# Optimization experiments

Hardware: AMD Instinct MI355X
Metric: run time of the kernel (lower is better)

The kernel has to match this reference:

```python
import jax, jax.numpy as jnp
import numpy as np

ALPHA = 0.2      # LeakyReLU negative slope
NEG_INF = -9e15  # mask value from the original module
EPS = 1e-8


def setup_inputs() -> dict:
    key = jax.random.key(0)
    k1, k2, k3, k4 = jax.random.split(key, 4)
    B, N, F_in, F_out = 8, 2048, 128, 64
    h = jax.random.normal(k1, (B, N, F_in), dtype=jnp.float32)
    u = jax.random.uniform(k2, (B, N, N), dtype=jnp.float32)
    adj = jnp.where(u > 0.9, u, 0.0)
    adj = jnp.maximum(adj, jnp.eye(N, dtype=jnp.float32)[None])
    # Xavier-uniform with gain 1.414 as in the torch init
    gain = 1.414
    bW = gain * np.sqrt(6.0 / (F_in + F_out))
    W = jax.random.uniform(k3, (F_in, F_out), jnp.float32, -bW, bW)
    ba = gain * np.sqrt(6.0 / (2 * F_out + 1))
    a = jax.random.uniform(k4, (2 * F_out, 1), jnp.float32, -ba, ba)
    return {"h": h, "adj": adj, "W": W, "a": a}


def reference(h, adj, W, a):
    # h: [B,N,Fin], adj: [B,N,N], W: [Fin,Fout], a: [2*Fout,1]
    F_out = W.shape[1]
    Wh = jnp.einsum('bnf,fo->bno', h, W)                      # [B,N,Fout]
    # Split-projection equivalent of cat([Wh_i, Wh_j]) @ a:
    # e[b,i,j] = leaky(Wh[b,i]@a1 + Wh[b,j]@a2)
    a1 = a[:F_out, 0]
    a2 = a[F_out:, 0]
    e = jax.nn.leaky_relu(
        (Wh @ a1)[:, :, None] + (Wh @ a2)[:, None, :],        # [B,N,N]
        negative_slope=ALPHA,
    )
    att = jnp.where(adj > 0, e, NEG_INF)
    att = jax.nn.softmax(att, axis=2)
    att = att * adj
    att = att / (jnp.sum(att, axis=2, keepdims=True) + EPS)
    h_prime = jnp.einsum('bij,bjo->bio', att, Wh)             # [B,N,Fout]
    return jax.nn.elu(h_prime)                                # concat=True -> ELU
```

## Files before the change

### kernel.cpp

```cpp
#include <hip/hip_runtime.h>
#include <hip/hip_bf16.h>
#include <stdint.h>

#define LRELU_ALPHA 0.2f

constexpr int BB = 8, NN = 2048, FIN = 128, FOUT = 64;
constexpr int GEMM_ROWS = 32;
constexpr int NBLK_G = BB * NN / GEMM_ROWS;

typedef __attribute__((ext_vector_type(8))) short short8;
typedef __attribute__((ext_vector_type(4))) float f32x4;
typedef __attribute__((ext_vector_type(2))) float f32x2;

__device__ __forceinline__ ushort bf16rn(float f) {
    __hip_bfloat16 h = __float2bfloat16(f);
    return *reinterpret_cast<ushort*>(&h);
}

#define HS 132
__global__ __launch_bounds__(256) void k_gemm_hw(const float* __restrict__ h,
                                                 const float* __restrict__ W,
                                                 const float* __restrict__ a,
                                                 ushort* __restrict__ WhP,
                                                 float* __restrict__ s1,
                                                 float* __restrict__ s2,
                                                 float* __restrict__ pmax) {
    __shared__ float hs[GEMM_ROWS * HS];
    __shared__ __align__(16) ushort fragbuf[2048];
    __shared__ float smax[16];
    const int tid = threadIdx.x;
    const int base = blockIdx.x * GEMM_ROWS;

    #pragma unroll
    for (int rep = 0; rep < 4; ++rep) {
        int flat4 = rep * 256 + tid;
        int row = flat4 >> 5, k4 = flat4 & 31;
        float4 v = *reinterpret_cast<const float4*>(h + (size_t)(base + row) * FIN + k4 * 4);
        *reinterpret_cast<float4*>(&hs[row * HS + k4 * 4]) = v;
    }
    __syncthreads();

    const int tr = tid >> 4;
    const int tc = tid & 15;
    float acc[2][4] = {};
    #pragma unroll 4
    for (int k = 0; k < FIN; ++k) {
        float4 wv = *reinterpret_cast<const float4*>(W + (size_t)k * FOUT + tc * 4);
        #pragma unroll
        for (int r = 0; r < 2; ++r) {
            float hv = hs[(tr * 2 + r) * HS + k];
            acc[r][0] = fmaf(hv, wv.x, acc[r][0]);
            acc[r][1] = fmaf(hv, wv.y, acc[r][1]);
            acc[r][2] = fmaf(hv, wv.z, acc[r][2]);
            acc[r][3] = fmaf(hv, wv.w, acc[r][3]);
        }
    }

    #pragma unroll
    for (int r = 0; r < 2; ++r) {
        const int jloc = tr * 2 + r;
        const int e = jloc & 7, kgrp = jloc >> 3;
        #pragma unroll
        for (int c = 0; c < 4; ++c) {
            const int col = tc * 4 + c;
            fragbuf[((col >> 4) * 64 + kgrp * 16 + (col & 15)) * 8 + e] = bf16rn(acc[r][c]);
        }
    }

    float a1c[4], a2c[4];
    #pragma unroll
    for (int c = 0; c < 4; ++c) {
        a1c[c] = a[tc * 4 + c];
        a2c[c] = a[FOUT + tc * 4 + c];
    }
    float maxp2 = -3.4e38f;
    #pragma unroll
    for (int r = 0; r < 2; ++r) {
        float p1 = acc[r][0] * a1c[0] + acc[r][1] * a1c[1] + acc[r][2] * a1c[2] + acc[r][3] * a1c[3];
        float p2 = acc[r][0] * a2c[0] + acc[r][1] * a2c[1] + acc[r][2] * a2c[2] + acc[r][3] * a2c[3];
        #pragma unroll
        for (int off = 1; off < 16; off <<= 1) {
            p1 += __shfl_xor(p1, off);
            p2 += __shfl_xor(p2, off);
        }
        if (tc == 0) {
            s1[base + tr * 2 + r] = p1;
            s2[base + tr * 2 + r] = p2;
            maxp2 = fmaxf(maxp2, p2);
        }
    }
    if (tc == 0) smax[tr] = maxp2;
    __syncthreads();

    const size_t region = ((size_t)((base >> 11) * 64 + ((base & 2047) >> 5))) * 2048;
    *reinterpret_cast<uint4*>(WhP + region + tid * 8) =
        *reinterpret_cast<const uint4*>(fragbuf + tid * 8);

    if (tid == 0) {
        float mm = smax[0];
        #pragma unroll
        for (int i = 1; i < 16; ++i) mm = fmaxf(mm, smax[i]);
        pmax[blockIdx.x] = mm;
    }
}

__device__ __forceinline__ uint32_t wvpk(float ax, float ay, float px, float py,
                                         float nx, float ny, float e1p, float e1n) {
    f32x2 t1 = f32x2{e1p, e1p} * f32x2{px, py};
    f32x2 t2 = f32x2{e1n, e1n} * f32x2{nx, ny};
    f32x2 mx = {fmaxf(t1.x, t2.x), fmaxf(t1.y, t2.y)};
    f32x2 w2 = f32x2{ax, ay} * mx;
    uint32_t u0 = __float_as_uint(w2.x) + 0x8000u;
    uint32_t u1 = __float_as_uint(w2.y) + 0x8000u;
    return __builtin_amdgcn_perm(u1, u0, 0x07060302);
}

__global__ __launch_bounds__(256, 4) void k_attn(const float* __restrict__ adj,
                                                 const ushort* __restrict__ WhP,
                                                 const float* __restrict__ s1,
                                                 const float* __restrict__ s2,
                                                 const float* __restrict__ pmax,
                                                 float* __restrict__ out) {
    __shared__ float e2p[NN];
    __shared__ float e2n[NN];
    __shared__ float lacc[4][16][68];
    __shared__ float lS[4][16];

    const int tid = threadIdx.x;
    const int l = tid & 63, w = tid >> 6;
    const int li = l & 15, lk = l >> 4;
    const int blk = blockIdx.x;
    const int b = blk >> 7;
    const int rowbase = blk * 16;
    const int row_i = rowbase + li;

    float m = -3.4e38f;
    #pragma unroll
    for (int t = 0; t < 8; ++t) m = fmaxf(m, pmax[l + 64 * t]);
    #pragma unroll
    for (int off = 32; off > 0; off >>= 1) m = fmaxf(m, __shfl_xor(m, off));

    const float* __restrict__ s2B = s2 + (size_t)b * NN;
    #pragma unroll
    for (int k = 0; k < 8; ++k) {
        const int j = k * 256 + tid;
        const float d = s2B[j] - m;
        e2p[j] = __expf(d);
        e2n[j] = __expf(LRELU_ALPHA * d);
    }

    const float s1i = s1[row_i];
    const float cp = s1i + m;
    const float e1p = __expf(0.8f * fminf(cp, 0.f));
    const float e1n = __expf(-0.8f * fmaxf(cp, 0.f));

    __syncthreads();

    const float* __restrict__ adjp = adj + (size_t)row_i * NN + w * 512 + lk * 8;
    const ushort* __restrict__ whp = WhP + (size_t)b * 131072 + (size_t)(w * 16) * 2048 + l * 8;
    const float* __restrict__ e2pw = e2p + w * 512 + lk * 8;
    const float* __restrict__ e2nw = e2n + w * 512 + lk * 8;

    f32x4 acc0 = {0.f, 0.f, 0.f, 0.f};
    f32x4 acc1 = {0.f, 0.f, 0.f, 0.f};
    f32x4 acc2 = {0.f, 0.f, 0.f, 0.f};
    f32x4 acc3 = {0.f, 0.f, 0.f, 0.f};
    f32x4 accS = {0.f, 0.f, 0.f, 0.f};
    short8 ones;
    #pragma unroll
    for (int e = 0; e < 8; ++e) ones[e] = (short)0x3F80;

    float4 a0 = *reinterpret_cast<const float4*>(adjp);
    float4 a1 = *reinterpret_cast<const float4*>(adjp + 4);
    short8 b0 = *reinterpret_cast<const short8*>(whp);
    short8 b1 = *reinterpret_cast<const short8*>(whp + 512);
    short8 b2 = *reinterpret_cast<const short8*>(whp + 1024);
    short8 b3 = *reinterpret_cast<const short8*>(whp + 1536);

    #pragma unroll 2
    for (int t = 0; t < 16; ++t) {
        const int tn = (t < 15) ? t + 1 : 15;
        float4 na0 = *reinterpret_cast<const float4*>(adjp + tn * 32);
        float4 na1 = *reinterpret_cast<const float4*>(adjp + tn * 32 + 4);
        const ushort* np = whp + tn * 2048;
        short8 nb0 = *reinterpret_cast<const short8*>(np);
        short8 nb1 = *reinterpret_cast<const short8*>(np + 512);
        short8 nb2 = *reinterpret_cast<const short8*>(np + 1024);
        short8 nb3 = *reinterpret_cast<const short8*>(np + 1536);

        const float4* pp = reinterpret_cast<const float4*>(e2pw + t * 32);
        const float4* nn = reinterpret_cast<const float4*>(e2nw + t * 32);
        const float4 p0 = pp[0], p1 = pp[1];
        const float4 n0 = nn[0], n1 = nn[1];

        const uint32_t pk0 = wvpk(a0.x, a0.y, p0.x, p0.y, n0.x, n0.y, e1p, e1n);
        const uint32_t pk1 = wvpk(a0.z, a0.w, p0.z, p0.w, n0.z, n0.w, e1p, e1n);
        const uint32_t pk2 = wvpk(a1.x, a1.y, p1.x, p1.y, n1.x, n1.y, e1p, e1n);
        const uint32_t pk3 = wvpk(a1.z, a1.w, p1.z, p1.w, n1.z, n1.w, e1p, e1n);
        int4 afw = make_int4((int)pk0, (int)pk1, (int)pk2, (int)pk3);
        short8 af = *reinterpret_cast<short8*>(&afw);

        acc0 = __builtin_amdgcn_mfma_f32_16x16x32_bf16(af, b0, acc0, 0, 0, 0);
        acc1 = __builtin_amdgcn_mfma_f32_16x16x32_bf16(af, b1, acc1, 0, 0, 0);
        acc2 = __builtin_amdgcn_mfma_f32_16x16x32_bf16(af, b2, acc2, 0, 0, 0);
        acc3 = __builtin_amdgcn_mfma_f32_16x16x32_bf16(af, b3, acc3, 0, 0, 0);
        accS = __builtin_amdgcn_mfma_f32_16x16x32_bf16(af, ones, accS, 0, 0, 0);

        a0 = na0; a1 = na1;
        b0 = nb0; b1 = nb1; b2 = nb2; b3 = nb3;
    }

    if (li == 0) {
        #pragma unroll
        for (int r = 0; r < 4; ++r) lS[w][lk * 4 + r] = accS[r];
    }
    #pragma unroll
    for (int r = 0; r < 4; ++r) {
        lacc[w][lk * 4 + r][0 * 16 + li] = acc0[r];
        lacc[w][lk * 4 + r][1 * 16 + li] = acc1[r];
        lacc[w][lk * 4 + r][2 * 16 + li] = acc2[r];
        lacc[w][lk * 4 + r][3 * 16 + li] = acc3[r];
    }
    __syncthreads();

    #pragma unroll
    for (int q = 0; q < 4; ++q) {
        const int idx = q * 256 + tid;
        const int row = idx >> 6, col = idx & 63;
        float v = lacc[0][row][col] + lacc[1][row][col] + lacc[2][row][col] + lacc[3][row][col];
        float S = lS[0][row] + lS[1][row] + lS[2][row] + lS[3][row];
        float o = v / S;
        o = o > 0.f ? o : expm1f(o);
        out[(size_t)(rowbase + row) * FOUT + col] = o;
    }
}

extern "C" void kernel_launch(void* const* d_in, const int* in_sizes, int n_in,
                              void* d_out, int out_size, void* d_ws, size_t ws_size,
                              hipStream_t stream) {
    (void)in_sizes; (void)n_in; (void)out_size; (void)ws_size;
    const float* h   = (const float*)d_in[0];
    const float* adj = (const float*)d_in[1];
    const float* W   = (const float*)d_in[2];
    const float* a   = (const float*)d_in[3];
    float* out = (float*)d_out;

    ushort* WhP = (ushort*)d_ws;
    float* s1w  = (float*)(WhP + (size_t)BB * NN * FOUT);
    float* s2w  = s1w + (size_t)BB * NN;
    float* pmaxw = s2w + (size_t)BB * NN;

    k_gemm_hw<<<NBLK_G, 256, 0, stream>>>(h, W, a, WhP, s1w, s2w, pmaxw);
    k_attn<<<BB * NN / 16, 256, 0, stream>>>(adj, WhP, s1w, s2w, pmaxw, out);
}
```

Baseline: 45.55 us.

## Process 32 rows per attention block and stagger start tile per block

Each attention block now handles two 16-row groups, so each loaded Wh tile and the exp tables built in shared memory serve twice as many rows. This halves the number of blocks and the per-block setup of the e2p/e2n tables. The loop start is also rotated per block so concurrent blocks hit different Wh and adj regions. The cost is more registers and LDS per block, which may reduce occupancy, and fewer blocks in flight.

```diff
diff --git a/kernel.cpp b/kernel.cpp
--- a/kernel.cpp
+++ b/kernel.cpp
@@ -123,16 +123,17 @@
                                                  float* __restrict__ out) {
     __shared__ float e2p[NN];
     __shared__ float e2n[NN];
-    __shared__ float lacc[4][16][68];
-    __shared__ float lS[4][16];
+    __shared__ float lacc[4][32][68];
+    __shared__ float lS[4][32];
 
     const int tid = threadIdx.x;
     const int l = tid & 63, w = tid >> 6;
     const int li = l & 15, lk = l >> 4;
     const int blk = blockIdx.x;
-    const int b = blk >> 7;
-    const int rowbase = blk * 16;
-    const int row_i = rowbase + li;
+    const int b = blk >> 6;
+    const int rowbase = blk * 32;
+    const int rowA = rowbase + li;
+    const int rowB = rowbase + 16 + li;
 
     float m = -3.4e38f;
     #pragma unroll
@@ -149,82 +150,111 @@
         e2n[j] = __expf(LRELU_ALPHA * d);
     }
 
-    const float s1i = s1[row_i];
-    const float cp = s1i + m;
-    const float e1p = __expf(0.8f * fminf(cp, 0.f));
-    const float e1n = __expf(-0.8f * fmaxf(cp, 0.f));
-
-    __syncthreads();
-
-    const float* __restrict__ adjp = adj + (size_t)row_i * NN + w * 512 + lk * 8;
+    const float cpA = s1[rowA] + m;
+    const float e1pA = __expf(0.8f * fminf(cpA, 0.f));
+    const float e1nA = __expf(-0.8f * fmaxf(cpA, 0.f));
+    const float cpB = s1[rowB] + m;
+    const float e1pB = __expf(0.8f * fminf(cpB, 0.f));
+    const float e1nB = __expf(-0.8f * fmaxf(cpB, 0.f));
+
+    __syncthreads();
+
+    const float* __restrict__ adjA = adj + (size_t)rowA * NN + w * 512 + lk * 8;
+    const float* __restrict__ adjB = adj + (size_t)rowB * NN + w * 512 + lk * 8;
     const ushort* __restrict__ whp = WhP + (size_t)b * 131072 + (size_t)(w * 16) * 2048 + l * 8;
     const float* __restrict__ e2pw = e2p + w * 512 + lk * 8;
     const float* __restrict__ e2nw = e2n + w * 512 + lk * 8;
 
-    f32x4 acc0 = {0.f, 0.f, 0.f, 0.f};
-    f32x4 acc1 = {0.f, 0.f, 0.f, 0.f};
-    f32x4 acc2 = {0.f, 0.f, 0.f, 0.f};
-    f32x4 acc3 = {0.f, 0.f, 0.f, 0.f};
-    f32x4 accS = {0.f, 0.f, 0.f, 0.f};
+    f32x4 acc0a = {0,0,0,0}, acc1a = {0,0,0,0}, acc2a = {0,0,0,0}, acc3a = {0,0,0,0};
+    f32x4 acc0b = {0,0,0,0}, acc1b = {0,0,0,0}, acc2b = {0,0,0,0}, acc3b = {0,0,0,0};
+    f32x4 accSa = {0,0,0,0}, accSb = {0,0,0,0};
     short8 ones;
     #pragma unroll
     for (int e = 0; e < 8; ++e) ones[e] = (short)0x3F80;
 
-    float4 a0 = *reinterpret_cast<const float4*>(adjp);
-    float4 a1 = *reinterpret_cast<const float4*>(adjp + 4);
-    short8 b0 = *reinterpret_cast<const short8*>(whp);
-    short8 b1 = *reinterpret_cast<const short8*>(whp + 512);
-    short8 b2 = *reinterpret_cast<const short8*>(whp + 1024);
-    short8 b3 = *reinterpret_cast<const short8*>(whp + 1536);
-
+    const int off0 = (blk * 5) & 15;
+
+    float4 aA0 = *reinterpret_cast<const float4*>(adjA + off0 * 32);
+    float4 aA1 = *reinterpret_cast<const float4*>(adjA + off0 * 32 + 4);
+    float4 aB0 = *reinterpret_cast<const float4*>(adjB + off0 * 32);
+    float4 aB1 = *reinterpret_cast<const float4*>(adjB + off0 * 32 + 4);
+    short8 b0 = *reinterpret_cast<const short8*>(whp + off0 * 2048);
+    short8 b1 = *reinterpret_cast<const short8*>(whp + off0 * 2048 + 512);
+    short8 b2 = *reinterpret_cast<const short8*>(whp + off0 * 2048 + 1024);
+    short8 b3 = *reinterpret_cast<const short8*>(whp + off0 * 2048 + 1536);
+
+    int tt = off0;
     #pragma unroll 2
     for (int t = 0; t < 16; ++t) {
-        const int tn = (t < 15) ? t + 1 : 15;
-        float4 na0 = *reinterpret_cast<const float4*>(adjp + tn * 32);
-        float4 na1 = *reinterpret_cast<const float4*>(adjp + tn * 32 + 4);
+        const int tn = (tt + 1) & 15;
+        float4 nA0 = *reinterpret_cast<const float4*>(adjA + tn * 32);
+        float4 nA1 = *reinterpret_cast<const float4*>(adjA + tn * 32 + 4);
+        float4 nB0 = *reinterpret_cast<const float4*>(adjB + tn * 32);
+        float4 nB1 = *reinterpret_cast<const float4*>(adjB + tn * 32 + 4);
         const ushort* np = whp + tn * 2048;
         short8 nb0 = *reinterpret_cast<const short8*>(np);
         short8 nb1 = *reinterpret_cast<const short8*>(np + 512);
         short8 nb2 = *reinterpret_cast<const short8*>(np + 1024);
         short8 nb3 = *reinterpret_cast<const short8*>(np + 1536);
 
-        const float4* pp = reinterpret_cast<const float4*>(e2pw + t * 32);
-        const float4* nn = reinterpret_cast<const float4*>(e2nw + t * 32);
+        const float4* pp = reinterpret_cast<const float4*>(e2pw + tt * 32);
+        const float4* nn = reinterpret_cast<const float4*>(e2nw + tt * 32);
         const float4 p0 = pp[0], p1 = pp[1];
         const float4 n0 = nn[0], n1 = nn[1];
 
-        const uint32_t pk0 = wvpk(a0.x, a0.y, p0.x, p0.y, n0.x, n0.y, e1p, e1n);
-        const uint32_t pk1 = wvpk(a0.z, a0.w, p0.z, p0.w, n0.z, n0.w, e1p, e1n);
-        const uint32_t pk2 = wvpk(a1.x, a1.y, p1.x, p1.y, n1.x, n1.y, e1p, e1n);
-        const uint32_t pk3 = wvpk(a1.z, a1.w, p1.z, p1.w, n1.z, n1.w, e1p, e1n);
-        int4 afw = make_int4((int)pk0, (int)pk1, (int)pk2, (int)pk3);
-        short8 af = *reinterpret_cast<short8*>(&afw);
-
-        acc0 = __builtin_amdgcn_mfma_f32_16x16x32_bf16(af, b0, acc0, 0, 0, 0);
-        acc1 = __builtin_amdgcn_mfma_f32_16x16x32_bf16(af, b1, acc1, 0, 0, 0);
-        acc2 = __builtin_amdgcn_mfma_f32_16x16x32_bf16(af, b2, acc2, 0, 0, 0);
-        acc3 = __builtin_amdgcn_mfma_f32_16x16x32_bf16(af, b3, acc3, 0, 0, 0);
-        accS = __builtin_amdgcn_mfma_f32_16x16x32_bf16(af, ones, accS, 0, 0, 0);
-
-        a0 = na0; a1 = na1;
+        uint32_t k0, k1, k2, k3;
+        k0 = wvpk(aA0.x, aA0.y, p0.x, p0.y, n0.x, n0.y, e1pA, e1nA);
+        k1 = wvpk(aA0.z, aA0.w, p0.z, p0.w, n0.z, n0.w, e1pA, e1nA);
+        k2 = wvpk(aA1.x, aA1.y, p1.x, p1.y, n1.x, n1.y, e1pA, e1nA);
+        k3 = wvpk(aA1.z, aA1.w, p1.z, p1.w, n1.z, n1.w, e1pA, e1nA);
+        int4 afwA = make_int4((int)k0, (int)k1, (int)k2, (int)k3);
+        short8 afA = *reinterpret_cast<short8*>(&afwA);
+
+        k0 = wvpk(aB0.x, aB0.y, p0.x, p0.y, n0.x, n0.y, e1pB, e1nB);
+        k1 = wvpk(aB0.z, aB0.w, p0.z, p0.w, n0.z, n0.w, e1pB, e1nB);
+        k2 = wvpk(aB1.x, aB1.y, p1.x, p1.y, n1.x, n1.y, e1pB, e1nB);
+        k3 = wvpk(aB1.z, aB1.w, p1.z, p1.w, n1.z, n1.w, e1pB, e1nB);
+        int4 afwB = make_int4((int)k0, (int)k1, (int)k2, (int)k3);
+        short8 afB = *reinterpret_cast<short8*>(&afwB);
+
+        acc0a = __builtin_amdgcn_mfma_f32_16x16x32_bf16(afA, b0, acc0a, 0, 0, 0);
+        acc0b = __builtin_amdgcn_mfma_f32_16x16x32_bf16(afB, b0, acc0b, 0, 0, 0);
+        acc1a = __builtin_amdgcn_mfma_f32_16x16x32_bf16(afA, b1, acc1a, 0, 0, 0);
+        acc1b = __builtin_amdgcn_mfma_f32_16x16x32_bf16(afB, b1, acc1b, 0, 0, 0);
+        acc2a = __builtin_amdgcn_mfma_f32_16x16x32_bf16(afA, b2, acc2a, 0, 0, 0);
+        acc2b = __builtin_amdgcn_mfma_f32_16x16x32_bf16(afB, b2, acc2b, 0, 0, 0);
+        acc3a = __builtin_amdgcn_mfma_f32_16x16x32_bf16(afA, b3, acc3a, 0, 0, 0);
+        acc3b = __builtin_amdgcn_mfma_f32_16x16x32_bf16(afB, b3, acc3b, 0, 0, 0);
+        accSa = __builtin_amdgcn_mfma_f32_16x16x32_bf16(afA, ones, accSa, 0, 0, 0);
+        accSb = __builtin_amdgcn_mfma_f32_16x16x32_bf16(afB, ones, accSb, 0, 0, 0);
+
+        aA0 = nA0; aA1 = nA1; aB0 = nB0; aB1 = nB1;
         b0 = nb0; b1 = nb1; b2 = nb2; b3 = nb3;
+        tt = tn;
     }
 
     if (li == 0) {
         #pragma unroll
-        for (int r = 0; r < 4; ++r) lS[w][lk * 4 + r] = accS[r];
+        for (int r = 0; r < 4; ++r) {
+            lS[w][lk * 4 + r] = accSa[r];
+            lS[w][16 + lk * 4 + r] = accSb[r];
+        }
     }
     #pragma unroll
     for (int r = 0; r < 4; ++r) {
-        lacc[w][lk * 4 + r][0 * 16 + li] = acc0[r];
-        lacc[w][lk * 4 + r][1 * 16 + li] = acc1[r];
-        lacc[w][lk * 4 + r][2 * 16 + li] = acc2[r];
-        lacc[w][lk * 4 + r][3 * 16 + li] = acc3[r];
-    }
-    __syncthreads();
-
-    #pragma unroll
-    for (int q = 0; q < 4; ++q) {
+        lacc[w][lk * 4 + r][0 * 16 + li] = acc0a[r];
+        lacc[w][lk * 4 + r][1 * 16 + li] = acc1a[r];
+        lacc[w][lk * 4 + r][2 * 16 + li] = acc2a[r];
+        lacc[w][lk * 4 + r][3 * 16 + li] = acc3a[r];
+        lacc[w][16 + lk * 4 + r][0 * 16 + li] = acc0b[r];
+        lacc[w][16 + lk * 4 + r][1 * 16 + li] = acc1b[r];
+        lacc[w][16 + lk * 4 + r][2 * 16 + li] = acc2b[r];
+        lacc[w][16 + lk * 4 + r][3 * 16 + li] = acc3b[r];
+    }
+    __syncthreads();
+
+    #pragma unroll
+    for (int q = 0; q < 8; ++q) {
         const int idx = q * 256 + tid;
         const int row = idx >> 6, col = idx & 63;
         float v = lacc[0][row][col] + lacc[1][row][col] + lacc[2][row][col] + lacc[3][row][col];
@@ -251,5 +281,5 @@
     float* pmaxw = s2w + (size_t)BB * NN;
 
     k_gemm_hw<<<NBLK_G, 256, 0, stream>>>(h, W, a, WhP, s1w, s2w, pmaxw);
-    k_attn<<<BB * NN / 16, 256, 0, stream>>>(adj, WhP, s1w, s2w, pmaxw, out);
-}
+    k_attn<<<BB * NN / 32, 256, 0, stream>>>(adj, WhP, s1w, s2w, pmaxw, out);
+}
```

Result: no change. 45.27 us (-0.6%).
